# Kernel tuning notes

Measured on AMD Instinct MI355X. Metric: run time of the kernel, lower is better.

Reference implementation:

```python
import jax, jax.numpy as jnp
import numpy as np

B, L, IN = 4, 2048, 64
D, N, K, NL, NC = 256, 16, 32, 2, 2


def _ln(x, g, b):
    m = x.mean(-1, keepdims=True)
    v = ((x - m) ** 2).mean(-1, keepdims=True)
    return (x - m) * jax.lax.rsqrt(v + 1e-5) * g + b


def _dwconv(x, w, b):
    # depthwise conv1d, kernel 3, padding 1; x: [B,L,D], w: [D,3]
    xp = jnp.pad(x, ((0, 0), (1, 1), (0, 0)))
    return xp[:, :-2] * w[:, 0] + xp[:, 1:-1] * w[:, 1] + xp[:, 2:] * w[:, 2] + b


def _ssm(x, loglam, wd, bd, wb, wc, wo, bo):
    # x: [B,L,D]
    lam = jax.nn.softplus(loglam)                      # [D,N]
    delta = jax.nn.softplus(x @ wd + bd)[..., None]    # [B,L,D,1]
    Bt = (x @ wb)[:, :, None, :]                       # [B,L,1,N]
    Ct = (x @ wc)[:, :, None, :]                       # [B,L,1,N]
    A_d = jnp.exp(-delta * lam)                        # [B,L,D,N]
    B_d = delta * Bt                                   # [B,L,D,N]
    A_l = jnp.moveaxis(A_d, 1, 0)                      # [L,B,D,N]
    B_l = jnp.moveaxis(B_d, 1, 0)

    def step(h, ab):
        a, b = ab
        h = a * h + b
        return h, h

    h0 = jnp.zeros((x.shape[0], D, N), x.dtype)
    _, hs = jax.lax.scan(step, h0, (A_l, B_l))         # [L,B,D,N]
    ys = hs * jnp.moveaxis(Ct, 1, 0)                   # [L,B,D,N]
    out = jnp.moveaxis(ys, 0, 1).reshape(x.shape[0], x.shape[1], D * N)
    return out @ wo + bo


def _temporal_block(x, lg, lb, cw, cb, loglam, wd, bd, wb, wc, wo, bo, gw, gb, pw, pb):
    res = x
    xn = _ln(x, lg, lb)
    xc = _dwconv(xn, cw, cb)
    xs = _ssm(xc, loglam, wd, bd, wb, wc, wo, bo)
    g = jax.nn.sigmoid(xn @ gw + gb)
    return (xs * g) @ pw + pb + res


def _spectral(x, fr, fi):
    X = jnp.fft.rfft(x, axis=1)                        # [B,F,D] complex64
    mag = jnp.abs(X).mean(axis=(0, 2))                 # [F]
    k = min(K, X.shape[1])
    _, idx = jax.lax.top_k(mag, k)
    filt = (fr[:, :k] + 1j * fi[:, :k]).T              # [k,D]
    Xk = X[:, idx, :] * filt[None]
    Xo = jnp.zeros(X.shape, X.dtype).at[:, idx, :].set(Xk)
    return jnp.fft.irfft(Xo, n=x.shape[1], axis=1)


def setup_inputs() -> dict:
    key = jax.random.key(0)
    ks = jax.random.split(key, 32)
    rn = lambda i, shape, s=0.02: jax.random.normal(ks[i], shape, jnp.float32) * s
    inp = {
        "x": jax.random.normal(ks[0], (B, L, IN), jnp.float32),
        "w_in": rn(1, (IN, D), 0.1), "b_in": jnp.zeros((D,), jnp.float32),
        "ln_g": jnp.ones((NL, D), jnp.float32), "ln_b": jnp.zeros((NL, D), jnp.float32),
        "conv_w": rn(2, (NL, D, 3), 0.3), "conv_b": jnp.zeros((NL, D), jnp.float32),
        "loglam": jax.random.uniform(ks[3], (NL, D, N), jnp.float32),
        "wd": rn(4, (NL, D, D), 0.05), "bd": jnp.zeros((NL, D), jnp.float32),
        "wb": rn(5, (NL, D, N), 0.05), "wc": rn(6, (NL, D, N), 0.05),
        "wo": rn(7, (NL, D * N, D), 0.01), "bo": jnp.zeros((NL, D), jnp.float32),
        "gate_w": rn(8, (NL, D, D), 0.05), "gate_b": jnp.zeros((NL, D), jnp.float32),
        "proj_w": rn(9, (NL, D, D), 0.05), "proj_b": jnp.zeros((NL, D), jnp.float32),
        "fr": rn(10, (D, K)), "fi": rn(11, (D, K)),
        "alpha": jnp.full((D,), 0.5, jnp.float32), "beta": jnp.full((D,), 0.5, jnp.float32),
        "g_out": jnp.ones((D,), jnp.float32), "b_out": jnp.zeros((D,), jnp.float32),
        "hw1": rn(12, (D, D // 2), 0.05), "hb1": jnp.zeros((D // 2,), jnp.float32),
        "hw2": rn(13, (D // 2, NC), 0.05), "hb2": jnp.zeros((NC,), jnp.float32),
    }
    return inp


def reference(x, w_in, b_in, ln_g, ln_b, conv_w, conv_b, loglam, wd, bd, wb, wc, wo, bo,
              gate_w, gate_b, proj_w, proj_b, fr, fi, alpha, beta, g_out, b_out,
              hw1, hb1, hw2, hb2):
    h = x @ w_in + b_in                                # [B,L,D]
    xt = h
    for i in range(NL):
        xt = _temporal_block(xt, ln_g[i], ln_b[i], conv_w[i], conv_b[i], loglam[i],
                             wd[i], bd[i], wb[i], wc[i], wo[i], bo[i],
                             gate_w[i], gate_b[i], proj_w[i], proj_b[i])
    xs = _spectral(h, fr, fi)
    z = alpha * xt + beta * xs
    z = _ln(z, g_out, b_out)
    zl = z[:, -1, :]                                   # [B,D]
    hid = jax.nn.silu(zl @ hw1 + hb1)                  # dropout is identity in eval
    return hid @ hw2 + hb2                             # [B,NC]
```

## Files before the change

### kernel.cpp

```cpp
#include <hip/hip_runtime.h>
#include <hip/hip_bf16.h>
#include <math.h>

#define BB   4
#define LL   2048
#define INF_ 64
#define DD   256
#define NN   16
#define KK   32
#define BLn  (BB*LL)
#define FCNT 1025
#define FSTR 1056
#define SKM  8192
#define SKN  256
#define PSZ  ((size_t)SKM * SKN)
#define IX(x) ((x) + ((x) >> 6))

typedef short short4v __attribute__((ext_vector_type(4)));
typedef short short8 __attribute__((ext_vector_type(8)));
typedef float f32x4  __attribute__((ext_vector_type(4)));

__device__ __forceinline__ float softplusf(float x) {
    return x > 20.f ? x : log1pf(__expf(x));
}
__device__ __forceinline__ float sigmoidf_(float x) {
    return 1.f / (1.f + __expf(-x));
}
__device__ __forceinline__ short bfs(float v) {
    __hip_bfloat16 h = __float2bfloat16(v);
    return *reinterpret_cast<short*>(&h);
}

__global__ void prep_kernel(const float* __restrict__ wd, const float* __restrict__ gw,
                            const float* __restrict__ pw, const float* __restrict__ wo,
                            const float* __restrict__ wb, const float* __restrict__ wc,
                            const float* __restrict__ w_in, float* __restrict__ tab,
                            __hip_bfloat16* __restrict__ cat0, __hip_bfloat16* __restrict__ cat1,
                            __hip_bfloat16* __restrict__ gwt, __hip_bfloat16* __restrict__ pwt,
                            __hip_bfloat16* __restrict__ wot, __hip_bfloat16* __restrict__ wint) {
    __shared__ float t[32][33];
    const int tid = threadIdx.x;
    int blk = blockIdx.x;
    if (blk < 8) {
        int i = blk * 256 + tid;
        if (i < 2048) {
            double ang = 2.0 * 3.14159265358979323846 * (double)i / 2048.0;
            tab[i]        = (float)cos(ang);
            tab[2048 + i] = (float)sin(ang);
        }
        return;
    }
    blk -= 8;
    const float* W; __hip_bfloat16* Wt; int K, N, bx, by;
    if (blk < 64)        { W = wd;                     Wt = cat0; K = 256;  N = 256; bx = blk & 7; by = blk >> 3; }
    else if (blk < 128)  { int q = blk - 64;  W = wd + 65536; Wt = cat1; K = 256; N = 256; bx = q & 7; by = q >> 3; }
    else if (blk < 192)  { int q = blk - 128; W = gw;  Wt = gwt;  K = 256;  N = 256; bx = q & 7; by = q >> 3; }
    else if (blk < 256)  { int q = blk - 192; W = pw;  Wt = pwt;  K = 256;  N = 256; bx = q & 7; by = q >> 3; }
    else if (blk < 1280) { int q = blk - 256; W = wo;  Wt = wot;  K = 4096; N = 256; bx = q & 7; by = q >> 3; }
    else if (blk < 1344) {
        int j = (blk - 1280) & 31;
        const float* src0 = (blk < 1312) ? wb : wb + DD * NN;
        const float* src1 = (blk < 1312) ? wc : wc + DD * NN;
        __hip_bfloat16* cat = (blk < 1312) ? cat0 : cat1;
        const float* src = (j < 16) ? src0 : src1;
        cat[(size_t)(256 + j) * 256 + tid] = __float2bfloat16(src[tid * 16 + (j & 15)]);
        return;
    } else { int q = blk - 1344; W = w_in; Wt = wint; K = 64; N = 256; bx = q & 7; by = q >> 3; }
    const int k0 = by * 32, n0 = bx * 32;
    if (k0 >= K) return;
    const int tx = tid & 31, ty = tid >> 5;
    for (int r = ty; r < 32; r += 8) t[r][tx] = W[(size_t)(k0 + r) * N + n0 + tx];
    __syncthreads();
    for (int r = ty; r < 32; r += 8)
        Wt[(size_t)(n0 + r) * K + k0 + tx] = __float2bfloat16(t[tx][r]);
}

__global__ __launch_bounds__(256)
void gemm_in_kernel(const float* __restrict__ x, const __hip_bfloat16* __restrict__ wint,
                    const float* __restrict__ b_in, float* __restrict__ h,
                    float* __restrict__ ht) {
    __shared__ alignas(16) short As[64][72];
    __shared__ alignas(16) short Bs[64][72];
    __shared__ float ts[64][68];
    const int tid = threadIdx.x;
    const int w = tid >> 6, lane = tid & 63;
    const int hi = lane >> 4, lo = lane & 15;
    const int row0 = blockIdx.y * 64, col0 = blockIdx.x * 64;
    const short* B = (const short*)wint;
#pragma unroll
    for (int e = 0; e < 4; ++e) {
        int q = e * 256 + tid;
        int r = q >> 4, c4 = (q & 15) * 4;
        float4 v = *(const float4*)&x[(size_t)(row0 + r) * 64 + c4];
        short4v s = {bfs(v.x), bfs(v.y), bfs(v.z), bfs(v.w)};
        *(short4v*)&As[r][c4] = s;
    }
#pragma unroll
    for (int e = 0; e < 2; ++e) {
        int q = e * 256 + tid;
        int r = q >> 3, c8 = (q & 7) * 8;
        *(short8*)&Bs[r][c8] = *(const short8*)&B[(size_t)(col0 + r) * 64 + c8];
    }
    __syncthreads();
    f32x4 acc[4];
    f32x4 zz = {0.f, 0.f, 0.f, 0.f};
#pragma unroll
    for (int n = 0; n < 4; ++n) acc[n] = zz;
#pragma unroll
    for (int s = 0; s < 2; ++s) {
        short8 af = *(const short8*)&As[w * 16 + lo][s * 32 + hi * 8];
#pragma unroll
        for (int n = 0; n < 4; ++n) {
            short8 bf = *(const short8*)&Bs[n * 16 + lo][s * 32 + hi * 8];
            acc[n] = __builtin_amdgcn_mfma_f32_16x16x32_bf16(af, bf, acc[n], 0, 0, 0);
        }
    }
#pragma unroll
    for (int n = 0; n < 4; ++n)
#pragma unroll
        for (int r = 0; r < 4; ++r) {
            const int row = row0 + w * 16 + hi * 4 + r;
            const int col = col0 + n * 16 + lo;
            float v = acc[n][r] + b_in[col];
            h[(size_t)row * 256 + col] = v;
            ts[n * 16 + lo][w * 16 + hi * 4 + r] = v;
        }
    __syncthreads();
    const int b = row0 >> 11, l0 = row0 & 2047, d0 = col0;
    const int dr = tid >> 2, seg = tid & 3;
    float* dst = ht + ((size_t)(b * 256 + d0 + dr)) * LL + l0 + seg * 16;
#pragma unroll
    for (int j = 0; j < 4; ++j)
        *(f32x4*)&dst[j * 4] = *(const f32x4*)&ts[dr][seg * 16 + j * 4];
}

__global__ __launch_bounds__(256)
void lnconv_kernel(const float* __restrict__ X, const float* __restrict__ g,
                   const float* __restrict__ bln, const float* __restrict__ cw,
                   const float* __restrict__ cb, __hip_bfloat16* __restrict__ xn_bf,
                   __hip_bfloat16* __restrict__ xc_bf) {
    __shared__ float xs[34][260];
    const int tid = threadIdx.x;
    const int w = tid >> 6, lane = tid & 63;
    const int blk = blockIdx.x;
    const int b = (blk * 32) >> 11, L0 = (blk * 32) & 2047;
    const float4 g4 = *(const float4*)&g[lane * 4];
    const float4 b4 = *(const float4*)&bln[lane * 4];
    for (int slot = w; slot < 34; slot += 4) {
        const int l = L0 - 1 + slot;
        if (l < 0 || l >= LL) {
            f32x4 z = {0.f, 0.f, 0.f, 0.f};
            *(f32x4*)&xs[slot][lane * 4] = z;
            continue;
        }
        float4 v = *(const float4*)&X[((size_t)b * LL + l) * DD + lane * 4];
        float s = v.x + v.y + v.z + v.w;
#pragma unroll
        for (int off = 1; off < 64; off <<= 1) s += __shfl_xor(s, off);
        float m = s * (1.f / DD);
        float cx = v.x - m, cy = v.y - m, cz = v.z - m, cw_ = v.w - m;
        float q = cx * cx + cy * cy + cz * cz + cw_ * cw_;
#pragma unroll
        for (int off = 1; off < 64; off <<= 1) q += __shfl_xor(q, off);
        float inv = rsqrtf(q * (1.f / DD) + 1e-5f);
        f32x4 y;
        y[0] = cx * inv * g4.x + b4.x;
        y[1] = cy * inv * g4.y + b4.y;
        y[2] = cz * inv * g4.z + b4.z;
        y[3] = cw_ * inv * g4.w + b4.w;
        *(f32x4*)&xs[slot][lane * 4] = y;
        if (slot >= 1 && slot <= 32) {
            short4v s4 = {bfs(y[0]), bfs(y[1]), bfs(y[2]), bfs(y[3])};
            *(short4v*)&xn_bf[((size_t)b * LL + l) * DD + lane * 4] = s4;
        }
    }
    __syncthreads();
    const int d = tid;
    const float w0 = cw[d * 3 + 0], w1 = cw[d * 3 + 1], w2 = cw[d * 3 + 2], cbd = cb[d];
    float xm = xs[0][d], x0 = xs[1][d];
    for (int rw = 0; rw < 32; ++rw) {
        float xp = xs[rw + 2][d];
        xc_bf[((size_t)b * LL + L0 + rw) * DD + d] =
            __float2bfloat16(fmaf(w0, xm, fmaf(w1, x0, fmaf(w2, xp, cbd))));
        xm = x0; x0 = xp;
    }
}

template<int MODE>
__global__ __launch_bounds__(256)
void gemm_core(const short* __restrict__ A, const short* __restrict__ Bw,
               const float* __restrict__ bias, const float* __restrict__ x1,
               const float* __restrict__ x2, float* __restrict__ o0,
               float* __restrict__ o1, float* __restrict__ o2,
               __hip_bfloat16* __restrict__ ob) {
    __shared__ alignas(16) short As[2][64][40];
    __shared__ alignas(16) short Bs[2][64][40];
    const int tid = threadIdx.x;
    const int w = tid >> 6, lane = tid & 63;
    const int hi = lane >> 4, lo = lane & 15;
    const int row0 = blockIdx.y * 64, col0 = blockIdx.x * 64;
    f32x4 acc[4];
    f32x4 zz = {0.f, 0.f, 0.f, 0.f};
#pragma unroll
    for (int n = 0; n < 4; ++n) acc[n] = zz;
    const int sr = tid >> 2, sc = (tid & 3) * 8;
    short8 pa = *(const short8*)&A[(size_t)(row0 + sr) * 256 + sc];
    short8 pb = *(const short8*)&Bw[(size_t)(col0 + sr) * 256 + sc];
    *(short8*)&As[0][sr][sc] = pa;
    *(short8*)&Bs[0][sr][sc] = pb;
    pa = *(const short8*)&A[(size_t)(row0 + sr) * 256 + 32 + sc];
    pb = *(const short8*)&Bw[(size_t)(col0 + sr) * 256 + 32 + sc];
    __syncthreads();
    int cur = 0;
    for (int it = 0; it < 8; ++it) {
        if (it + 1 < 8) {
            *(short8*)&As[cur ^ 1][sr][sc] = pa;
            *(short8*)&Bs[cur ^ 1][sr][sc] = pb;
        }
        if (it + 2 < 8) {
            const int k0 = (it + 2) << 5;
            pa = *(const short8*)&A[(size_t)(row0 + sr) * 256 + k0 + sc];
            pb = *(const short8*)&Bw[(size_t)(col0 + sr) * 256 + k0 + sc];
        }
        short8 af = *(const short8*)&As[cur][w * 16 + lo][hi * 8];
        short8 bfr[4];
#pragma unroll
        for (int n = 0; n < 4; ++n)
            bfr[n] = *(const short8*)&Bs[cur][n * 16 + lo][hi * 8];
#pragma unroll
        for (int n = 0; n < 4; ++n)
            acc[n] = __builtin_amdgcn_mfma_f32_16x16x32_bf16(af, bfr[n], acc[n], 0, 0, 0);
        __syncthreads();
        cur ^= 1;
    }
#pragma unroll
    for (int n = 0; n < 4; ++n) {
#pragma unroll
        for (int r = 0; r < 4; ++r) {
            const int row = row0 + w * 16 + hi * 4 + r;
            const int col = col0 + n * 16 + lo;
            float v = acc[n][r];
            if constexpr (MODE == 0) {
                if (col < 256)      o0[(size_t)row * 256 + col] = softplusf(v + bias[col]);
                else if (col < 272) o1[(size_t)row * 16 + col - 256] = v;
                else if (col < 288) o2[(size_t)row * 16 + col - 272] = v;
            } else if constexpr (MODE == 1) {
                float gv = sigmoidf_(v + bias[col]);
                size_t idx = (size_t)row * 256 + col;
                float s = x1[idx] + x1[PSZ + idx] + x1[2 * PSZ + idx] + x1[3 * PSZ + idx] + x2[col];
                ob[idx] = __float2bfloat16(gv * s);
            } else {
                o0[(size_t)row * 256 + col] = v + bias[col] + x1[(size_t)row * 256 + col];
            }
        }
    }
}

__global__ __launch_bounds__(256)
void gemm_sk_kernel(const __hip_bfloat16* __restrict__ Abf, const __hip_bfloat16* __restrict__ Wt,
                    float* __restrict__ P) {
    __shared__ alignas(16) short As[2][128][40];
    __shared__ alignas(16) short Bs[2][64][40];
    const int tid = threadIdx.x;
    const int f = blockIdx.x;
    const int xcd = f & 7, slot = f >> 3;
    const int col = slot & 3;
    const int rk = xcd + (slot >> 2) * 8;
    const int row = rk & 63, kb = rk >> 6;
    const int row0 = row * 128, col0 = col * 64;
    const size_t kbase = (size_t)kb * 1024;
    const int w = tid >> 6, lane = tid & 63;
    const int hi = lane >> 4, lo = lane & 15;
    const short* A = (const short*)Abf;
    const short* B = (const short*)Wt;
    f32x4 acc[2][4];
    f32x4 zz = {0.f, 0.f, 0.f, 0.f};
#pragma unroll
    for (int m = 0; m < 2; ++m)
#pragma unroll
        for (int n = 0; n < 4; ++n) acc[m][n] = zz;
    const int ra0 = tid >> 2,          ca0 = (tid & 3) * 8;
    const int ra1 = (256 + tid) >> 2,  ca1 = ((256 + tid) & 3) * 8;
    short8 pa0 = *(const short8*)&A[(size_t)(row0 + ra0) * 4096 + kbase + ca0];
    short8 pa1 = *(const short8*)&A[(size_t)(row0 + ra1) * 4096 + kbase + ca1];
    short8 pb  = *(const short8*)&B[(size_t)(col0 + ra0) * 4096 + kbase + ca0];
    *(short8*)&As[0][ra0][ca0] = pa0;
    *(short8*)&As[0][ra1][ca1] = pa1;
    *(short8*)&Bs[0][ra0][ca0] = pb;
    pa0 = *(const short8*)&A[(size_t)(row0 + ra0) * 4096 + kbase + 32 + ca0];
    pa1 = *(const short8*)&A[(size_t)(row0 + ra1) * 4096 + kbase + 32 + ca1];
    pb  = *(const short8*)&B[(size_t)(col0 + ra0) * 4096 + kbase + 32 + ca0];
    __syncthreads();
    int cur = 0;
    for (int it = 0; it < 32; ++it) {
        if (it + 1 < 32) {
            *(short8*)&As[cur ^ 1][ra0][ca0] = pa0;
            *(short8*)&As[cur ^ 1][ra1][ca1] = pa1;
            *(short8*)&Bs[cur ^ 1][ra0][ca0] = pb;
        }
        if (it + 2 < 32) {
            const size_t k0 = kbase + ((it + 2) << 5);
            pa0 = *(const short8*)&A[(size_t)(row0 + ra0) * 4096 + k0 + ca0];
            pa1 = *(const short8*)&A[(size_t)(row0 + ra1) * 4096 + k0 + ca1];
            pb  = *(const short8*)&B[(size_t)(col0 + ra0) * 4096 + k0 + ca0];
        }
        short8 af[2], bfr[4];
#pragma unroll
        for (int m = 0; m < 2; ++m)
            af[m] = *(const short8*)&As[cur][w * 32 + m * 16 + lo][hi * 8];
#pragma unroll
        for (int n = 0; n < 4; ++n)
            bfr[n] = *(const short8*)&Bs[cur][n * 16 + lo][hi * 8];
#pragma unroll
        for (int m = 0; m < 2; ++m)
#pragma unroll
            for (int n = 0; n < 4; ++n)
                acc[m][n] = __builtin_amdgcn_mfma_f32_16x16x32_bf16(af[m], bfr[n], acc[m][n], 0, 0, 0);
        __syncthreads();
        cur ^= 1;
    }
    float* Pk = P + (size_t)kb * PSZ;
#pragma unroll
    for (int m = 0; m < 2; ++m)
#pragma unroll
        for (int n = 0; n < 4; ++n)
#pragma unroll
            for (int r = 0; r < 4; ++r) {
                int rr = row0 + w * 32 + m * 16 + hi * 4 + r;
                int cc = col0 + n * 16 + lo;
                Pk[(size_t)rr * SKN + cc] = acc[m][n][r];
            }
}

template<int PHASE>
__global__ void ssm_chunk_kernel(const float* __restrict__ delta, const float* __restrict__ Bt,
                                 const float* __restrict__ Ct, const float* __restrict__ loglam,
                                 float* __restrict__ sA, float* __restrict__ sB,
                                 __hip_bfloat16* __restrict__ ys) {
    __shared__ float dl[128][16];
    __shared__ float btl[128][16];
    __shared__ float ctl[128][16];
    const int dblk = blockIdx.x, c = blockIdx.y, b = blockIdx.z;
    const int tid = threadIdx.x;
    const size_t lbase = (size_t)b * LL + c * 128;
    for (int i = tid; i < 2048; i += 256) {
        int l = i >> 4, q = i & 15;
        dl[l][q]  = delta[(lbase + l) * DD + dblk * 16 + q];
        btl[l][q] = Bt[(lbase + l) * NN + q];
        if (PHASE == 1) ctl[l][q] = Ct[(lbase + l) * NN + q];
    }
    float hv = 0.f, ap = 1.f;
    if (PHASE == 1) {
        for (int cc = 0; cc < c; ++cc) {
            size_t oi = ((size_t)(b * 16 + cc)) * 4096 + dblk * 256 + tid;
            hv = fmaf(sA[oi], hv, sB[oi]);
        }
    }
    __syncthreads();
    const int dloc = tid >> 4, n = tid & 15;
    const float lam = softplusf(loglam[(dblk * 16 + dloc) * NN + n]);
    for (int l = 0; l < 128; ++l) {
        float dv = dl[l][dloc];
        float a = __expf(-dv * lam);
        hv = fmaf(a, hv, dv * btl[l][n]);
        if (PHASE == 0) ap *= a;
        else ys[(lbase + l) * (DD * NN) + dblk * 256 + tid] = __float2bfloat16(hv * ctl[l][n]);
    }
    if (PHASE == 0) {
        size_t oi = ((size_t)(b * 16 + c)) * 4096 + dblk * 256 + tid;
        sA[oi] = ap; sB[oi] = hv;
    }
}

__global__ void last_ssm_part_kernel(const float* __restrict__ sA, const float* __restrict__ sB,
                                     const float* __restrict__ Ct,
                                     const float* __restrict__ wo, float* __restrict__ part) {
    __shared__ float hC[4][128];
    const int c = blockIdx.x, tid = threadIdx.x;
    const int p0 = c * 128;
#pragma unroll
    for (int e = 0; e < 2; ++e) {
        int i = e * 256 + tid;
        int b = i >> 7, p = i & 127;
        float hh = 0.f;
#pragma unroll
        for (int cc = 0; cc < 16; ++cc) {
            size_t oi = ((size_t)(b * 16 + cc)) * 4096 + p0 + p;
            hh = fmaf(sA[oi], hh, sB[oi]);
        }
        hC[b][p] = hh * Ct[((size_t)b * LL + (LL - 1)) * NN + (p & 15)];
    }
    __syncthreads();
    float a0 = 0.f, a1 = 0.f, a2 = 0.f, a3 = 0.f;
    for (int p = 0; p < 128; ++p) {
        float wv = wo[(size_t)(p0 + p) * DD + tid];
        a0 = fmaf(hC[0][p], wv, a0);
        a1 = fmaf(hC[1][p], wv, a1);
        a2 = fmaf(hC[2][p], wv, a2);
        a3 = fmaf(hC[3][p], wv, a3);
    }
    part[(0 * 32 + c) * DD + tid] = a0;
    part[(1 * 32 + c) * DD + tid] = a1;
    part[(2 * 32 + c) * DD + tid] = a2;
    part[(3 * 32 + c) * DD + tid] = a3;
}

__global__ void last_redproj_kernel(const float* __restrict__ part, const float* __restrict__ bo,
                                    const __hip_bfloat16* __restrict__ xn, const float* __restrict__ gw,
                                    const float* __restrict__ gb, const float* __restrict__ pw,
                                    const float* __restrict__ pb, const float* __restrict__ resid,
                                    float* __restrict__ xtlast) {
    __shared__ float xrow[256];
    __shared__ float xsg[256];
    const int b = blockIdx.x, d = threadIdx.x;
    float ol = bo[d];
#pragma unroll
    for (int c = 0; c < 32; ++c) ol += part[(b * 32 + c) * DD + d];
    const size_t rbase = ((size_t)b * LL + (LL - 1)) * DD;
    xrow[d] = __bfloat162float(xn[rbase + d]);
    __syncthreads();
    float acc = gb[d];
    for (int k = 0; k < 256; ++k) acc = fmaf(xrow[k], gw[(size_t)k * DD + d], acc);
    xsg[d] = ol * sigmoidf_(acc);
    __syncthreads();
    float acc2 = pb[d];
    for (int k = 0; k < 256; ++k) acc2 = fmaf(xsg[k], pw[(size_t)k * DD + d], acc2);
    xtlast[b * DD + d] = acc2 + resid[rbase + d];
}

__global__ __launch_bounds__(256)
void fft2_kernel(const float* __restrict__ ht, const float* __restrict__ tab,
                 float* __restrict__ Xre, float* __restrict__ Xim) {
    __shared__ float re[2080];
    __shared__ float im[2080];
    __shared__ float c2[2048];
    __shared__ float s2[2048];
    const int tid = threadIdx.x;
    const int pair = blockIdx.x;
    const int b = pair >> 7, d0 = pair & 127;
    for (int p = tid; p < 2048; p += 256) {
        if (p >= 1) {
            int lh = 31 - __clz((unsigned)p);
            int j = p - (1 << lh);
            int t = j << (10 - lh);
            c2[p] = tab[t]; s2[p] = tab[2048 + t];
        }
    }
    const float* ha = ht + ((size_t)b * 256 + d0) * LL;
    const float* hb = ha + (size_t)128 * LL;
    for (int i = tid; i < 2048; i += 256) {
        int r = (int)(__brev((unsigned)i) >> 21);
        re[IX(r)] = ha[i];
        im[IX(r)] = hb[i];
    }
    __syncthreads();
#pragma unroll
    for (int s = 1; s <= 11; ++s) {
        const int half = 1 << (s - 1);
#pragma unroll
        for (int e = 0; e < 4; ++e) {
            int q = e * 256 + tid;
            int j = q & (half - 1);
            int i0 = ((q >> (s - 1)) << s) + j;
            int i1 = i0 + half;
            float wr = c2[half + j], wi = -s2[half + j];
            float xr = re[IX(i1)], xi = im[IX(i1)];
            float tr = xr * wr - xi * wi;
            float ti = xr * wi + xi * wr;
            float ur = re[IX(i0)], ui = im[IX(i0)];
            re[IX(i0)] = ur + tr; im[IX(i0)] = ui + ti;
            re[IX(i1)] = ur - tr; im[IX(i1)] = ui - ti;
        }
        __syncthreads();
    }
    const int seqa = b * 256 + d0;
    float* xra = Xre + (size_t)seqa * FSTR;
    float* xia = Xim + (size_t)seqa * FSTR;
    float* xrb = xra + (size_t)128 * FSTR;
    float* xib = xia + (size_t)128 * FSTR;
    for (int f = tid; f < FCNT; f += 256) {
        int nf = (2048 - f) & 2047;
        float zrf = re[IX(f)], zif = im[IX(f)];
        float zrn = re[IX(nf)], zin = im[IX(nf)];
        xra[f] = 0.5f * (zrf + zrn);
        xia[f] = 0.5f * (zif - zin);
        xrb[f] = 0.5f * (zif + zin);
        xib[f] = 0.5f * (zrn - zrf);
    }
}

__global__ void mag_part_kernel(const float* __restrict__ Xre, const float* __restrict__ Xim,
                                float* __restrict__ part) {
    const int fb = blockIdx.x, sb = blockIdx.y;
    const int tid = threadIdx.x;
    const int f = fb * 256 + tid;
    float s = 0.f;
    if (f < FCNT) {
        for (int q = 0; q < 64; ++q) {
            size_t base = (size_t)(sb * 64 + q) * FSTR + f;
            float re = Xre[base], im = Xim[base];
            s += sqrtf(re * re + im * im);
        }
    }
    part[sb * 1280 + fb * 256 + tid] = s;
}

__global__ void topk_kernel(const float* __restrict__ part, int* __restrict__ sel) {
    __shared__ float vals[1280];
    __shared__ float wv[4];
    __shared__ int wi[4];
    const int tid = threadIdx.x;
    const int lane = tid & 63, wid = tid >> 6;
    for (int i = tid; i < 1280; i += 256) {
        float v = -1e30f;
        if (i < FCNT) {
            v = 0.f;
#pragma unroll
            for (int sb = 0; sb < 16; ++sb) v += part[sb * 1280 + i];
        }
        vals[i] = v;
    }
    __syncthreads();
    for (int k = 0; k < 32; ++k) {
        float bv = -1e30f; int bi = 0x7fffffff;
        for (int i = tid; i < FCNT; i += 256) {
            float v = vals[i];
            if (v > bv) { bv = v; bi = i; }
        }
#pragma unroll
        for (int off = 32; off > 0; off >>= 1) {
            float ov = __shfl_down(bv, off);
            int   oi = __shfl_down(bi, off);
            if (ov > bv || (ov == bv && oi < bi)) { bv = ov; bi = oi; }
        }
        if (lane == 0) { wv[wid] = bv; wi[wid] = bi; }
        __syncthreads();
        if (tid == 0) {
            float fv = wv[0]; int fi = wi[0];
#pragma unroll
            for (int q = 1; q < 4; ++q)
                if (wv[q] > fv || (wv[q] == fv && wi[q] < fi)) { fv = wv[q]; fi = wi[q]; }
            sel[k] = fi;
            vals[fi] = -1e30f;
        }
        __syncthreads();
    }
}

__global__ void head_kernel(const float* __restrict__ Xre, const float* __restrict__ Xim,
                            const int* __restrict__ sel, const float* __restrict__ fr,
                            const float* __restrict__ fi, const float* __restrict__ tab,
                            const float* __restrict__ xtlast,
                            const float* __restrict__ alpha, const float* __restrict__ beta,
                            const float* __restrict__ gout, const float* __restrict__ bout,
                            const float* __restrict__ hw1, const float* __restrict__ hb1,
                            const float* __restrict__ hw2, const float* __restrict__ hb2,
                            float* __restrict__ out) {
    __shared__ float red[256];
    __shared__ float z[256];
    __shared__ float hid[128];
    const int b = blockIdx.x, tid = threadIdx.x;
    const size_t sbase = (size_t)(b * 256 + tid) * FSTR;
    float xsl = 0.f;
    for (int j = 0; j < 32; ++j) {
        int f = sel[j];
        float xr = Xre[sbase + f];
        float xi = Xim[sbase + f];
        float frv = fr[tid * KK + j], fiv = fi[tid * KK + j];
        float xor_ = xr * frv - xi * fiv;
        float xoi  = xr * fiv + xi * frv;
        int kk2 = (f * (LL - 1)) & (LL - 1);
        float c = tab[kk2], s = tab[2048 + kk2];
        float w = (f == 0 || f == 1024) ? 1.f : 2.f;
        xsl = fmaf(w, xor_ * c - xoi * s, xsl);
    }
    xsl *= (1.f / LL);
    float zv = alpha[tid] * xtlast[b * 256 + tid] + beta[tid] * xsl;
    red[tid] = zv; __syncthreads();
    for (int s = 128; s > 0; s >>= 1) { if (tid < s) red[tid] += red[tid + s]; __syncthreads(); }
    float m = red[0] * (1.f / DD);
    __syncthreads();
    float c = zv - m;
    red[tid] = c * c; __syncthreads();
    for (int s = 128; s > 0; s >>= 1) { if (tid < s) red[tid] += red[tid + s]; __syncthreads(); }
    float var = red[0] * (1.f / DD);
    z[tid] = c * rsqrtf(var + 1e-5f) * gout[tid] + bout[tid];
    __syncthreads();
    if (tid < 128) {
        float a = hb1[tid];
        for (int k = 0; k < 256; ++k) a = fmaf(z[k], hw1[(size_t)k * 128 + tid], a);
        hid[tid] = a * sigmoidf_(a);
    }
    __syncthreads();
    if (tid < 2) {
        float a = hb2[tid];
        for (int k = 0; k < 128; ++k) a = fmaf(hid[k], hw2[(size_t)k * 2 + tid], a);
        out[b * 2 + tid] = a;
    }
}

extern "C" void kernel_launch(void* const* d_in, const int* in_sizes, int n_in,
                              void* d_out, int out_size, void* d_ws, size_t ws_size,
                              hipStream_t stream) {
    const float* x      = (const float*)d_in[0];
    const float* w_in   = (const float*)d_in[1];
    const float* b_in   = (const float*)d_in[2];
    const float* ln_g   = (const float*)d_in[3];
    const float* ln_b   = (const float*)d_in[4];
    const float* conv_w = (const float*)d_in[5];
    const float* conv_b = (const float*)d_in[6];
    const float* loglam = (const float*)d_in[7];
    const float* wd     = (const float*)d_in[8];
    const float* bd     = (const float*)d_in[9];
    const float* wb     = (const float*)d_in[10];
    const float* wc     = (const float*)d_in[11];
    const float* wo     = (const float*)d_in[12];
    const float* bo     = (const float*)d_in[13];
    const float* gw     = (const float*)d_in[14];
    const float* gb     = (const float*)d_in[15];
    const float* pw     = (const float*)d_in[16];
    const float* pb     = (const float*)d_in[17];
    const float* fr     = (const float*)d_in[18];
    const float* fi     = (const float*)d_in[19];
    const float* alpha  = (const float*)d_in[20];
    const float* beta   = (const float*)d_in[21];
    const float* gout   = (const float*)d_in[22];
    const float* bout   = (const float*)d_in[23];
    const float* hw1    = (const float*)d_in[24];
    const float* hb1    = (const float*)d_in[25];
    const float* hw2    = (const float*)d_in[26];
    const float* hb2    = (const float*)d_in[27];

    float* ws = (float*)d_ws;
    size_t o = 0;
    auto alloc = [&](size_t n) { float* p = ws + o; o += (n + 15) & ~(size_t)15; return p; };

    const size_t BLnDD = (size_t)BLn * DD;
    float* h      = alloc(BLnDD);
    float* xt1    = alloc(BLnDD);
    float* ht     = alloc(BLnDD);
    float* delta  = alloc(BLnDD);
    float* Pbuf   = alloc(4 * PSZ);
    float* Btm    = alloc((size_t)BLn * NN);
    float* Ctm    = alloc((size_t)BLn * NN);
    float* tab    = alloc(4096);
    float* ysf    = alloc(BLnDD * NN / 2);
    float* sA     = alloc((size_t)BB * 16 * 4096);
    float* sB     = alloc((size_t)BB * 16 * 4096);
    float* xnbf_f = alloc(BLnDD / 2);
    float* xcbf_f = alloc(BLnDD / 2);
    float* xsgf   = alloc(BLnDD / 2);
    float* cat0_f = alloc((size_t)320 * 256 / 2);
    float* cat1_f = alloc((size_t)320 * 256 / 2);
    float* gwt_f  = alloc((size_t)DD * DD / 2);
    float* pwt_f  = alloc((size_t)DD * DD / 2);
    float* wot_f  = alloc((size_t)DD * NN * DD / 2);
    float* wint_f = alloc((size_t)DD * 64 / 2);
    float* magp   = alloc(16 * 1280);
    int*   sel    = (int*)alloc(32);
    float* lpart  = alloc((size_t)BB * 32 * DD);
    float* xtlast = alloc(BB * DD);

    __hip_bfloat16* ys    = (__hip_bfloat16*)ysf;
    float*          Xre   = ysf;
    float*          Xim   = ysf + (size_t)1024 * FSTR;
    __hip_bfloat16* xn_bf = (__hip_bfloat16*)xnbf_f;
    __hip_bfloat16* xc_bf = (__hip_bfloat16*)xcbf_f;
    __hip_bfloat16* xsg_bf= (__hip_bfloat16*)xsgf;
    __hip_bfloat16* cat0  = (__hip_bfloat16*)cat0_f;
    __hip_bfloat16* cat1  = (__hip_bfloat16*)cat1_f;
    __hip_bfloat16* gwt   = (__hip_bfloat16*)gwt_f;
    __hip_bfloat16* pwt   = (__hip_bfloat16*)pwt_f;
    __hip_bfloat16* wot   = (__hip_bfloat16*)wot_f;
    __hip_bfloat16* wint  = (__hip_bfloat16*)wint_f;

    const dim3 blk(256);

    prep_kernel<<<1368, blk, 0, stream>>>(wd, gw, pw, wo, wb, wc, w_in, tab,
                                          cat0, cat1, gwt, pwt, wot, wint);
    gemm_in_kernel<<<dim3(4, 128), blk, 0, stream>>>(x, wint, b_in, h, ht);

    const dim3 qgrid(5, BLn / 64);
    const dim3 ggrid(4, BLn / 64);
    const dim3 sgrid(16, 16, BB);

    lnconv_kernel<<<BLn / 32, blk, 0, stream>>>(h, ln_g, ln_b, conv_w, conv_b, xn_bf, xc_bf);
    gemm_core<0><<<qgrid, blk, 0, stream>>>((const short*)xc_bf, (const short*)cat0,
                                            bd, nullptr, nullptr, delta, Btm, Ctm, nullptr);
    ssm_chunk_kernel<0><<<sgrid, blk, 0, stream>>>(delta, Btm, nullptr, loglam,
                                                   sA, sB, nullptr);
    ssm_chunk_kernel<1><<<sgrid, blk, 0, stream>>>(delta, Btm, Ctm, loglam,
                                                   sA, sB, ys);
    gemm_sk_kernel<<<1024, blk, 0, stream>>>(ys, wot, Pbuf);
    gemm_core<1><<<ggrid, blk, 0, stream>>>((const short*)xn_bf, (const short*)gwt,
                                            gb, Pbuf, bo, nullptr, nullptr, nullptr, xsg_bf);
    gemm_core<2><<<ggrid, blk, 0, stream>>>((const short*)xsg_bf, (const short*)pwt,
                                            pb, h, nullptr, xt1, nullptr, nullptr, nullptr);

    lnconv_kernel<<<BLn / 32, blk, 0, stream>>>(xt1, ln_g + DD, ln_b + DD,
                                                conv_w + DD * 3, conv_b + DD, xn_bf, xc_bf);
    gemm_core<0><<<qgrid, blk, 0, stream>>>((const short*)xc_bf, (const short*)cat1,
                                            bd + DD, nullptr, nullptr, delta, Btm, Ctm, nullptr);
    ssm_chunk_kernel<0><<<sgrid, blk, 0, stream>>>(delta, Btm, nullptr, loglam + DD * NN,
                                                   sA, sB, nullptr);
    last_ssm_part_kernel<<<32, blk, 0, stream>>>(sA, sB, Ctm, wo + (size_t)DD * NN * DD, lpart);
    last_redproj_kernel<<<BB, blk, 0, stream>>>(lpart, bo + DD, xn_bf,
                                                gw + (size_t)DD * DD, gb + DD,
                                                pw + (size_t)DD * DD, pb + DD, xt1, xtlast);

    fft2_kernel<<<512, blk, 0, stream>>>(ht, tab, Xre, Xim);
    mag_part_kernel<<<dim3(5, 16), blk, 0, stream>>>(Xre, Xim, magp);
    topk_kernel<<<1, blk, 0, stream>>>(magp, sel);

    head_kernel<<<BB, blk, 0, stream>>>(Xre, Xim, sel, fr, fi, tab, xtlast,
                                        alpha, beta, gout, bout,
                                        hw1, hb1, hw2, hb2, (float*)d_out);
}
```

Before: 282.1 us.

## Halve split-K partitions in output GEMM and single-wave top-k selection

The split-K GEMM for the D*N→D projection now uses 64-row tiles and two K splits of 2048 instead of 128-row tiles and four splits of 1024, so the consumer epilogue sums two partial buffers instead of four and the partial buffer shrinks. The block count stays the same but each block does a longer K loop with less register accumulation. Separately, top-k selection runs in a single wavefront using shuffles, removing per-iteration block barriers. The risk is a longer serial K loop per block and less A-tile reuse. Launch-side grid changes are not shown, so consistency depends on the unseen grid size.

After: 297.3 us. 5.4% more time.

```diff
diff --git a/kernel.cpp b/kernel.cpp
--- a/kernel.cpp
+++ b/kernel.cpp
@@ -247,7 +247,7 @@
             } else if constexpr (MODE == 1) {
                 float gv = sigmoidf_(v + bias[col]);
                 size_t idx = (size_t)row * 256 + col;
-                float s = x1[idx] + x1[PSZ + idx] + x1[2 * PSZ + idx] + x1[3 * PSZ + idx] + x2[col];
+                float s = x1[idx] + x1[PSZ + idx] + x2[col];
                 ob[idx] = __float2bfloat16(gv * s);
             } else {
                 o0[(size_t)row * 256 + col] = v + bias[col] + x1[(size_t)row * 256 + col];
@@ -259,77 +259,63 @@
 __global__ __launch_bounds__(256)
 void gemm_sk_kernel(const __hip_bfloat16* __restrict__ Abf, const __hip_bfloat16* __restrict__ Wt,
                     float* __restrict__ P) {
-    __shared__ alignas(16) short As[2][128][40];
+    __shared__ alignas(16) short As[2][64][40];
     __shared__ alignas(16) short Bs[2][64][40];
     const int tid = threadIdx.x;
     const int f = blockIdx.x;
-    const int xcd = f & 7, slot = f >> 3;
-    const int col = slot & 3;
-    const int rk = xcd + (slot >> 2) * 8;
-    const int row = rk & 63, kb = rk >> 6;
-    const int row0 = row * 128, col0 = col * 64;
-    const size_t kbase = (size_t)kb * 1024;
+    const int xcd = f & 7, s = f >> 3;
+    const int col = s & 3, u = s >> 2;
+    const int rowkb = xcd + u * 8;
+    const int row = rowkb & 127, kb = rowkb >> 7;
+    const int row0 = row * 64, col0 = col * 64;
+    const size_t kbase = (size_t)kb * 2048;
     const int w = tid >> 6, lane = tid & 63;
     const int hi = lane >> 4, lo = lane & 15;
     const short* A = (const short*)Abf;
     const short* B = (const short*)Wt;
-    f32x4 acc[2][4];
+    f32x4 acc[4];
     f32x4 zz = {0.f, 0.f, 0.f, 0.f};
 #pragma unroll
-    for (int m = 0; m < 2; ++m)
-#pragma unroll
-        for (int n = 0; n < 4; ++n) acc[m][n] = zz;
-    const int ra0 = tid >> 2,          ca0 = (tid & 3) * 8;
-    const int ra1 = (256 + tid) >> 2,  ca1 = ((256 + tid) & 3) * 8;
-    short8 pa0 = *(const short8*)&A[(size_t)(row0 + ra0) * 4096 + kbase + ca0];
-    short8 pa1 = *(const short8*)&A[(size_t)(row0 + ra1) * 4096 + kbase + ca1];
-    short8 pb  = *(const short8*)&B[(size_t)(col0 + ra0) * 4096 + kbase + ca0];
-    *(short8*)&As[0][ra0][ca0] = pa0;
-    *(short8*)&As[0][ra1][ca1] = pa1;
-    *(short8*)&Bs[0][ra0][ca0] = pb;
-    pa0 = *(const short8*)&A[(size_t)(row0 + ra0) * 4096 + kbase + 32 + ca0];
-    pa1 = *(const short8*)&A[(size_t)(row0 + ra1) * 4096 + kbase + 32 + ca1];
-    pb  = *(const short8*)&B[(size_t)(col0 + ra0) * 4096 + kbase + 32 + ca0];
+    for (int n = 0; n < 4; ++n) acc[n] = zz;
+    const int sr = tid >> 2, sc = (tid & 3) * 8;
+    short8 pa = *(const short8*)&A[(size_t)(row0 + sr) * 4096 + kbase + sc];
+    short8 pb = *(const short8*)&B[(size_t)(col0 + sr) * 4096 + kbase + sc];
+    *(short8*)&As[0][sr][sc] = pa;
+    *(short8*)&Bs[0][sr][sc] = pb;
+    pa = *(const short8*)&A[(size_t)(row0 + sr) * 4096 + kbase + 32 + sc];
+    pb = *(const short8*)&B[(size_t)(col0 + sr) * 4096 + kbase + 32 + sc];
     __syncthreads();
     int cur = 0;
-    for (int it = 0; it < 32; ++it) {
-        if (it + 1 < 32) {
-            *(short8*)&As[cur ^ 1][ra0][ca0] = pa0;
-            *(short8*)&As[cur ^ 1][ra1][ca1] = pa1;
-            *(short8*)&Bs[cur ^ 1][ra0][ca0] = pb;
-        }
-        if (it + 2 < 32) {
+    for (int it = 0; it < 64; ++it) {
+        if (it + 1 < 64) {
+            *(short8*)&As[cur ^ 1][sr][sc] = pa;
+            *(short8*)&Bs[cur ^ 1][sr][sc] = pb;
+        }
+        if (it + 2 < 64) {
             const size_t k0 = kbase + ((it + 2) << 5);
-            pa0 = *(const short8*)&A[(size_t)(row0 + ra0) * 4096 + k0 + ca0];
-            pa1 = *(const short8*)&A[(size_t)(row0 + ra1) * 4096 + k0 + ca1];
-            pb  = *(const short8*)&B[(size_t)(col0 + ra0) * 4096 + k0 + ca0];
-        }
-        short8 af[2], bfr[4];
-#pragma unroll
-        for (int m = 0; m < 2; ++m)
-            af[m] = *(const short8*)&As[cur][w * 32 + m * 16 + lo][hi * 8];
+            pa = *(const short8*)&A[(size_t)(row0 + sr) * 4096 + k0 + sc];
+            pb = *(const short8*)&B[(size_t)(col0 + sr) * 4096 + k0 + sc];
+        }
+        short8 af = *(const short8*)&As[cur][w * 16 + lo][hi * 8];
+        short8 bfr[4];
 #pragma unroll
         for (int n = 0; n < 4; ++n)
             bfr[n] = *(const short8*)&Bs[cur][n * 16 + lo][hi * 8];
 #pragma unroll
-        for (int m = 0; m < 2; ++m)
-#pragma unroll
-            for (int n = 0; n < 4; ++n)
-                acc[m][n] = __builtin_amdgcn_mfma_f32_16x16x32_bf16(af[m], bfr[n], acc[m][n], 0, 0, 0);
+        for (int n = 0; n < 4; ++n)
+            acc[n] = __builtin_amdgcn_mfma_f32_16x16x32_bf16(af, bfr[n], acc[n], 0, 0, 0);
         __syncthreads();
         cur ^= 1;
     }
     float* Pk = P + (size_t)kb * PSZ;
 #pragma unroll
-    for (int m = 0; m < 2; ++m)
-#pragma unroll
-        for (int n = 0; n < 4; ++n)
-#pragma unroll
-            for (int r = 0; r < 4; ++r) {
-                int rr = row0 + w * 32 + m * 16 + hi * 4 + r;
-                int cc = col0 + n * 16 + lo;
-                Pk[(size_t)rr * SKN + cc] = acc[m][n][r];
-            }
+    for (int n = 0; n < 4; ++n)
+#pragma unroll
+        for (int r = 0; r < 4; ++r) {
+            int rr = row0 + w * 16 + hi * 4 + r;
+            int cc = col0 + n * 16 + lo;
+            Pk[(size_t)rr * SKN + cc] = acc[n][r];
+        }
 }
 
 template<int PHASE>
@@ -507,10 +493,7 @@
 
 __global__ void topk_kernel(const float* __restrict__ part, int* __restrict__ sel) {
     __shared__ float vals[1280];
-    __shared__ float wv[4];
-    __shared__ int wi[4];
-    const int tid = threadIdx.x;
-    const int lane = tid & 63, wid = tid >> 6;
+    const int tid = threadIdx.x;
     for (int i = tid; i < 1280; i += 256) {
         float v = -1e30f;
         if (i < FCNT) {
@@ -521,9 +504,11 @@
         vals[i] = v;
     }
     __syncthreads();
+    if (tid >= 64) return;
+    const int lane = tid;
     for (int k = 0; k < 32; ++k) {
         float bv = -1e30f; int bi = 0x7fffffff;
-        for (int i = tid; i < FCNT; i += 256) {
+        for (int i = lane; i < 1280; i += 64) {
             float v = vals[i];
             if (v > bv) { bv = v; bi = i; }
         }
@@ -533,17 +518,9 @@
             int   oi = __shfl_down(bi, off);
             if (ov > bv || (ov == bv && oi < bi)) { bv = ov; bi = oi; }
         }
-        if (lane == 0) { wv[wid] = bv; wi[wid] = bi; }
-        __syncthreads();
-        if (tid == 0) {
-            float fv = wv[0]; int fi = wi[0];
-#pragma unroll
-            for (int q = 1; q < 4; ++q)
-                if (wv[q] > fv || (wv[q] == fv && wi[q] < fi)) { fv = wv[q]; fi = wi[q]; }
-            sel[k] = fi;
-            vals[fi] = -1e30f;
-        }
-        __syncthreads();
+        bi = __shfl(bi, 0);
+        if (lane == 0) sel[k] = bi;
+        vals[bi] = -1e30f;
     }
 }
 
@@ -640,7 +617,7 @@
     float* xt1    = alloc(BLnDD);
     float* ht     = alloc(BLnDD);
     float* delta  = alloc(BLnDD);
-    float* Pbuf   = alloc(4 * PSZ);
+    float* Pbuf   = alloc(2 * PSZ);
     float* Btm    = alloc((size_t)BLn * NN);
     float* Ctm    = alloc((size_t)BLn * NN);
     float* tab    = alloc(4096);
```
